# Performance work log

Hardware: AMD Instinct MI355X
Metric: run time of the kernel (lower is better)

## Reference

```python
import jax, jax.numpy as jnp
import numpy as np

NH, NKV, HD = 16, 4, 64  # num_heads, num_kv_heads, head_dim
ROPE_BASE = 10000.0


def setup_inputs() -> dict:
    key = jax.random.key(0)
    ks = jax.random.split(key, 5)
    B, S, D = 2, 2048, 1024
    x = jax.random.normal(ks[0], (B, S, D), dtype=jnp.float32)
    # torch Linear layout: [out_features, in_features], xavier-ish scale
    Wq = jax.random.normal(ks[1], (NH * HD, D), dtype=jnp.float32) * 0.02
    Wk = jax.random.normal(ks[2], (NKV * HD, D), dtype=jnp.float32) * 0.02
    Wv = jax.random.normal(ks[3], (NKV * HD, D), dtype=jnp.float32) * 0.02
    Wo = jax.random.normal(ks[4], (D, NH * HD), dtype=jnp.float32) * 0.02
    return {"x": x, "Wq": Wq, "Wk": Wk, "Wv": Wv, "Wo": Wo}


def _rotate_half(t):
    t1, t2 = jnp.split(t, 2, axis=-1)
    return jnp.concatenate([-t2, t1], axis=-1)


def _rope_cos_sin(seq_len, dtype):
    inv_freq = 1.0 / (ROPE_BASE ** (jnp.arange(0, HD, 2, dtype=jnp.float32) / HD))
    freqs = jnp.outer(jnp.arange(seq_len, dtype=jnp.float32), inv_freq)  # [S, HD/2]
    emb = jnp.concatenate([freqs, freqs], axis=-1)                       # [S, HD]
    return jnp.cos(emb).astype(dtype), jnp.sin(emb).astype(dtype)


def reference(x, Wq, Wk, Wv, Wo):
    B, S, D = x.shape
    scale = 1.0 / np.sqrt(HD)
    # projections (torch Linear: y = x @ W.T)
    q = jnp.einsum('bsd,ed->bse', x, Wq).reshape(B, S, NH, HD).transpose(0, 2, 1, 3)
    k = jnp.einsum('bsd,ed->bse', x, Wk).reshape(B, S, NKV, HD).transpose(0, 2, 1, 3)
    v = jnp.einsum('bsd,ed->bse', x, Wv).reshape(B, S, NKV, HD).transpose(0, 2, 1, 3)
    # RoPE
    cos, sin = _rope_cos_sin(S, x.dtype)
    cos = cos[None, None]  # [1,1,S,HD]
    sin = sin[None, None]
    q = q * cos + _rotate_half(q) * sin
    k = k * cos + _rotate_half(k) * sin
    # GQA: repeat kv heads (matches expand+reshape: head h = kvh*rep + r)
    rep = NH // NKV
    k = jnp.repeat(k, rep, axis=1)  # [B,NH,S,HD]
    v = jnp.repeat(v, rep, axis=1)
    # scaled dot-product attention, causal
    scores = jnp.einsum('bhqd,bhkd->bhqk', q, k) * scale
    causal = jnp.triu(jnp.ones((S, S), dtype=bool), k=1)
    scores = jnp.where(causal, jnp.float32(-jnp.inf), scores)
    attn = jax.nn.softmax(scores.astype(jnp.float32), axis=-1).astype(q.dtype)
    out = jnp.einsum('bhqk,bhkd->bhqd', attn, v)
    out = out.transpose(0, 2, 1, 3).reshape(B, S, NH * HD)
    return jnp.einsum('bse,de->bsd', out, Wo)
```

## Files before the change

### kernel.cpp

```cpp
#include <hip/hip_runtime.h>
#include <hip/hip_bf16.h>
#include <math.h>

#define B_    2
#define S_    2048
#define D_    1024
#define NH_   16
#define NKV_  4
#define HD_   64
#define NTOK  (B_ * S_)
#define QKVN  (NH_ * HD_ + 2 * NKV_ * HD_)
#define REP   (NH_ / NKV_)

typedef __attribute__((ext_vector_type(8))) short short8;
typedef __attribute__((ext_vector_type(4))) float f32x4;

__device__ short  g_xb[(size_t)NTOK * D_];
__device__ short  g_wqkv[(size_t)QKVN * D_];
__device__ short  g_wob[(size_t)D_ * NH_ * HD_];
__device__ float  g_yqkv[(size_t)NTOK * QKVN];
__device__ short  g_qb[(size_t)B_ * NH_  * S_ * HD_];
__device__ short  g_kb[(size_t)B_ * NKV_ * S_ * HD_];
__device__ short  g_vt[(size_t)B_ * NKV_ * HD_ * S_];
__device__ short  g_ao[(size_t)NTOK * NH_ * HD_];

static __device__ inline short f2bf(float f) {
  __hip_bfloat16 h = __float2bfloat16(f);
  return *reinterpret_cast<short*>(&h);
}

#define NX4   (NTOK * D_ / 4)
#define NWQ4  (NH_ * HD_ * D_ / 4)
#define NWK4  (NKV_ * HD_ * D_ / 4)
#define NWV4  NWK4
#define NWO4  (D_ * NH_ * HD_ / 4)
#define NCVT  (NX4 + NWQ4 + NWK4 + NWV4 + NWO4)

__global__ __launch_bounds__(256) void convert_all(const float* __restrict__ x,
                                                   const float* __restrict__ wq,
                                                   const float* __restrict__ wk,
                                                   const float* __restrict__ wv,
                                                   const float* __restrict__ wo) {
  int i = blockIdx.x * blockDim.x + threadIdx.x;
  if (i >= NCVT) return;
  const float* src; short* dst; int off;
  if (i < NX4)                          { src = x;  dst = g_xb;   off = i; }
  else if (i < NX4 + NWQ4)              { src = wq; dst = g_wqkv; off = i - NX4; }
  else if (i < NX4 + NWQ4 + NWK4)       { src = wk; dst = g_wqkv + (size_t)NWQ4 * 4;          off = i - NX4 - NWQ4; }
  else if (i < NX4 + NWQ4 + NWK4 + NWV4){ src = wv; dst = g_wqkv + (size_t)(NWQ4 + NWK4) * 4; off = i - NX4 - NWQ4 - NWK4; }
  else                                  { src = wo; dst = g_wob;  off = i - NX4 - NWQ4 - NWK4 - NWV4; }
  float4 v = ((const float4*)src)[off];
  short4 s;
  s.x = f2bf(v.x); s.y = f2bf(v.y); s.z = f2bf(v.z); s.w = f2bf(v.w);
  ((short4*)dst)[off] = s;
}

__global__ __launch_bounds__(256) void gemm_qkv() {
  const int w = threadIdx.x >> 6, lane = threadIdx.x & 63;
  const int m0 = blockIdx.x * 128 + w * 32;
  const int n0 = blockIdx.y * 64;
  const int lr = lane & 15, lk = (lane >> 4) * 8;

  f32x4 acc[2][4] = {};
  for (int k0 = 0; k0 < D_; k0 += 32) {
    short8 a0 = *(const short8*)(g_xb + (size_t)(m0 + lr) * D_ + k0 + lk);
    short8 a1 = *(const short8*)(g_xb + (size_t)(m0 + 16 + lr) * D_ + k0 + lk);
#pragma unroll
    for (int bj = 0; bj < 4; ++bj) {
      short8 bf = *(const short8*)(g_wqkv + (size_t)(n0 + bj * 16 + lr) * D_ + k0 + lk);
      acc[0][bj] = __builtin_amdgcn_mfma_f32_16x16x32_bf16(a0, bf, acc[0][bj], 0, 0, 0);
      acc[1][bj] = __builtin_amdgcn_mfma_f32_16x16x32_bf16(a1, bf, acc[1][bj], 0, 0, 0);
    }
  }
  const int rb = (lane >> 4) * 4;
#pragma unroll
  for (int af = 0; af < 2; ++af)
#pragma unroll
    for (int bj = 0; bj < 4; ++bj)
#pragma unroll
      for (int r = 0; r < 4; ++r)
        g_yqkv[(size_t)(m0 + af * 16 + rb + r) * QKVN + n0 + bj * 16 + lr] =
            acc[af][bj][r];
}

__global__ void rope_scatter() {
  int idx = blockIdx.x * blockDim.x + threadIdx.x;
  if (idx >= NTOK * (NH_ + NKV_) * 32) return;
  const int d    = idx & 31;
  const int head = (idx >> 5) % (NH_ + NKV_);
  const int tok  = idx / ((NH_ + NKV_) * 32);
  const int b = tok / S_, s = tok % S_;

  const float* src;
  short* dst;
  float qscale;
  if (head < NH_) {
    src = g_yqkv + (size_t)tok * QKVN + head * HD_;
    dst = g_qb + (((size_t)(b * NH_ + head)) * S_ + s) * HD_;
    qscale = 0.125f;
  } else {
    const int kvh = head - NH_;
    src = g_yqkv + (size_t)tok * QKVN + NH_ * HD_ + kvh * HD_;
    dst = g_kb + (((size_t)(b * NKV_ + kvh)) * S_ + s) * HD_;
    qscale = 1.0f;
  }
  const float x1 = src[d], x2 = src[d + 32];
  const float inv = exp2f((float)d * (-13.287712379549449f / 32.0f));
  const float ang = (float)s * inv;
  float sn, cs;
  sincosf(ang, &sn, &cs);
  dst[d]      = f2bf((x1 * cs - x2 * sn) * qscale);
  dst[d + 32] = f2bf((x2 * cs + x1 * sn) * qscale);
}

__global__ void vt_scatter() {
  int idx = blockIdx.x * blockDim.x + threadIdx.x;
  if (idx >= B_ * NKV_ * HD_ * S_) return;
  const int s   = idx & (S_ - 1);
  const int d   = (idx >> 11) & 63;
  const int kvh = (idx >> 17) & 3;
  const int b   = idx >> 19;
  const float v = g_yqkv[(size_t)(b * S_ + s) * QKVN + NH_ * HD_ + NKV_ * HD_ + kvh * HD_ + d];
  g_vt[(((size_t)(b * NKV_ + kvh)) * HD_ + d) * S_ + s] = f2bf(v);
}

__global__ __launch_bounds__(256) void attn_mfma() {
  const int bh  = blockIdx.x;
  const int b   = bh >> 4, h = bh & 15;
  const int kvh = h >> 2;
  const int qt  = (int)(gridDim.y - 1 - blockIdx.y);
  const int w   = threadIdx.x >> 6;
  const int lane = threadIdx.x & 63;
  const int g = lane >> 4, l = lane & 15;
  const int q0 = qt * 64 + w * 16;
  const int q_glob = q0 + l;

  const short* Qb = g_qb + ((size_t)bh * S_ + q0) * HD_;
  const short* Kb = g_kb + ((size_t)(b * NKV_ + kvh)) * S_ * HD_;
  const short* Vt = g_vt + ((size_t)(b * NKV_ + kvh)) * HD_ * S_;

  short8 qf[2];
  qf[0] = *(const short8*)(Qb + l * HD_ + g * 8);
  qf[1] = *(const short8*)(Qb + l * HD_ + 32 + g * 8);

  f32x4 o[4] = {};
  float m_run = -1e30f, l_run = 0.0f;

  const int nt = (q0 >> 5) + 1;
  for (int t = 0; t < nt; ++t) {
    f32x4 st[2] = {};
    const short* Kt = Kb + (size_t)(t * 32) * HD_;
#pragma unroll
    for (int ks = 0; ks < 2; ++ks) {
      short8 k0 = *(const short8*)(Kt + l * HD_ + ks * 32 + g * 8);
      short8 k1 = *(const short8*)(Kt + (16 + l) * HD_ + ks * 32 + g * 8);
      st[0] = __builtin_amdgcn_mfma_f32_16x16x32_bf16(k0, qf[ks], st[0], 0, 0, 0);
      st[1] = __builtin_amdgcn_mfma_f32_16x16x32_bf16(k1, qf[ks], st[1], 0, 0, 0);
    }
    float sv[2][4];
    float mt = -1e30f;
#pragma unroll
    for (int mf = 0; mf < 2; ++mf)
#pragma unroll
      for (int r = 0; r < 4; ++r) {
        const int kv = t * 32 + mf * 16 + g * 4 + r;
        float s = st[mf][r];
        s = (kv > q_glob) ? -1e30f : s;
        sv[mf][r] = s;
        mt = fmaxf(mt, s);
      }
    mt = fmaxf(mt, __shfl_xor(mt, 16, 64));
    mt = fmaxf(mt, __shfl_xor(mt, 32, 64));
    const float m_new = fmaxf(m_run, mt);
    const float alpha = __expf(m_run - m_new);
    float p[2][4];
    float ls = 0.0f;
#pragma unroll
    for (int mf = 0; mf < 2; ++mf)
#pragma unroll
      for (int r = 0; r < 4; ++r) {
        const float pv = __expf(sv[mf][r] - m_new);
        p[mf][r] = pv;
        ls += pv;
      }
    ls += __shfl_xor(ls, 16, 64);
    ls += __shfl_xor(ls, 32, 64);
    l_run = l_run * alpha + ls;
    m_run = m_new;
#pragma unroll
    for (int df = 0; df < 4; ++df)
#pragma unroll
      for (int r = 0; r < 4; ++r) o[df][r] *= alpha;

    short8 pt;
#pragma unroll
    for (int j = 0; j < 8; ++j) {
      const int src = l + ((lane >> 4 & 1) << 5) + ((j >> 2) << 4);
      const float v0 = __shfl(p[0][j & 3], src, 64);
      const float v1 = __shfl(p[1][j & 3], src, 64);
      pt[j] = f2bf((g & 2) ? v1 : v0);
    }
#pragma unroll
    for (int df = 0; df < 4; ++df) {
      short8 vf = *(const short8*)(Vt + (size_t)(df * 16 + l) * S_ + t * 32 + g * 8);
      o[df] = __builtin_amdgcn_mfma_f32_16x16x32_bf16(vf, pt, o[df], 0, 0, 0);
    }
  }

  const float inv_l = 1.0f / l_run;
  short* optr = g_ao + ((size_t)(b * S_ + q_glob)) * (NH_ * HD_) + h * HD_;
#pragma unroll
  for (int df = 0; df < 4; ++df) {
    short4 s4;
    s4.x = f2bf(o[df][0] * inv_l);
    s4.y = f2bf(o[df][1] * inv_l);
    s4.z = f2bf(o[df][2] * inv_l);
    s4.w = f2bf(o[df][3] * inv_l);
    *(short4*)(optr + df * 16 + g * 4) = s4;
  }
}

__global__ __launch_bounds__(256) void gemm_out(float* __restrict__ out) {
  const int w = threadIdx.x >> 6, lane = threadIdx.x & 63;
  const int m0 = blockIdx.x * 128 + w * 32;
  const int n0 = blockIdx.y * 64;
  const int lr = lane & 15, lk = (lane >> 4) * 8;
  const int K = NH_ * HD_;

  f32x4 acc[2][4] = {};
  for (int k0 = 0; k0 < K; k0 += 32) {
    short8 a0 = *(const short8*)(g_ao + (size_t)(m0 + lr) * K + k0 + lk);
    short8 a1 = *(const short8*)(g_ao + (size_t)(m0 + 16 + lr) * K + k0 + lk);
#pragma unroll
    for (int bj = 0; bj < 4; ++bj) {
      short8 bf = *(const short8*)(g_wob + (size_t)(n0 + bj * 16 + lr) * K + k0 + lk);
      acc[0][bj] = __builtin_amdgcn_mfma_f32_16x16x32_bf16(a0, bf, acc[0][bj], 0, 0, 0);
      acc[1][bj] = __builtin_amdgcn_mfma_f32_16x16x32_bf16(a1, bf, acc[1][bj], 0, 0, 0);
    }
  }
  const int rb = (lane >> 4) * 4;
#pragma unroll
  for (int af = 0; af < 2; ++af)
#pragma unroll
    for (int bj = 0; bj < 4; ++bj)
#pragma unroll
      for (int r = 0; r < 4; ++r)
        out[(size_t)(m0 + af * 16 + rb + r) * D_ + n0 + bj * 16 + lr] =
            acc[af][bj][r];
}

extern "C" void kernel_launch(void* const* d_in, const int* in_sizes, int n_in,
                              void* d_out, int out_size, void* d_ws, size_t ws_size,
                              hipStream_t stream) {
  const float* x  = (const float*)d_in[0];
  const float* Wq = (const float*)d_in[1];
  const float* Wk = (const float*)d_in[2];
  const float* Wv = (const float*)d_in[3];
  const float* Wo = (const float*)d_in[4];
  float* out = (float*)d_out;

  convert_all<<<(NCVT + 255) / 256, 256, 0, stream>>>(x, Wq, Wk, Wv, Wo);
  {
    dim3 g(NTOK / 128, QKVN / 64);
    gemm_qkv<<<g, 256, 0, stream>>>();
  }
  {
    int n = NTOK * (NH_ + NKV_) * 32;
    rope_scatter<<<(n + 255) / 256, 256, 0, stream>>>();
  }
  {
    int n = B_ * NKV_ * HD_ * S_;
    vt_scatter<<<(n + 255) / 256, 256, 0, stream>>>();
  }
  {
    dim3 g(B_ * NH_, S_ / 64);
    attn_mfma<<<g, 256, 0, stream>>>();
  }
  {
    dim3 g(NTOK / 128, D_ / 64);
    gemm_out<<<g, 256, 0, stream>>>(out);
  }
}
```

Measured before the change: 358.5 us.

## Fuse RoPE and V-transpose into QKV GEMM epilogue, restructure attention softmax

Removes the fp32 QKV intermediate buffer and the separate rope/vt scatter kernels by applying RoPE (from a precomputed cos/sin table) and writing bf16 Q, K and transposed V directly in the GEMM epilogue. The attention kernel now runs one wave per block over 16 queries. It also folds log2e into the Q scale so it can use exp2, skips the rescale when the running max has not grown by more than a threshold, defers the row-sum reduction to the end, packs P into bf16 pairs to halve the shuffles, and prefetches K/V fragments. This cuts memory traffic and launch count, at the cost of scattered epilogue stores and a slightly different numeric path from the lazy rescaling.

```diff
diff --git a/kernel.cpp b/kernel.cpp
--- a/kernel.cpp
+++ b/kernel.cpp
@@ -12,13 +12,16 @@
 #define QKVN  (NH_ * HD_ + 2 * NKV_ * HD_)
 #define REP   (NH_ / NKV_)
 
+#define LOG2E 1.4426950408889634f
+
 typedef __attribute__((ext_vector_type(8))) short short8;
 typedef __attribute__((ext_vector_type(4))) float f32x4;
 
 __device__ short  g_xb[(size_t)NTOK * D_];
 __device__ short  g_wqkv[(size_t)QKVN * D_];
 __device__ short  g_wob[(size_t)D_ * NH_ * HD_];
-__device__ float  g_yqkv[(size_t)NTOK * QKVN];
+__device__ float  g_rc[(size_t)S_ * 32];
+__device__ float  g_rs[(size_t)S_ * 32];
 __device__ short  g_qb[(size_t)B_ * NH_  * S_ * HD_];
 __device__ short  g_kb[(size_t)B_ * NKV_ * S_ * HD_];
 __device__ short  g_vt[(size_t)B_ * NKV_ * HD_ * S_];
@@ -27,6 +30,9 @@
 static __device__ inline short f2bf(float f) {
   __hip_bfloat16 h = __float2bfloat16(f);
   return *reinterpret_cast<short*>(&h);
+}
+static __device__ inline unsigned pack2(float lo, float hi) {
+  return ((unsigned)(unsigned short)f2bf(hi) << 16) | (unsigned)(unsigned short)f2bf(lo);
 }
 
 #define NX4   (NTOK * D_ / 4)
@@ -55,10 +61,22 @@
   ((short4*)dst)[off] = s;
 }
 
-__global__ __launch_bounds__(256) void gemm_qkv() {
+__global__ __launch_bounds__(256) void rope_tbl() {
+  int i = blockIdx.x * blockDim.x + threadIdx.x;
+  if (i >= S_ * 32) return;
+  const int d = i & 31, s = i >> 5;
+  const float inv = exp2f((float)d * (-13.287712379549449f / 32.0f));
+  const float ang = (float)s * inv;
+  float sn, cs;
+  sincosf(ang, &sn, &cs);
+  g_rc[i] = cs; g_rs[i] = sn;
+}
+
+__global__ __launch_bounds__(256) void gemm_qkv_rope() {
   const int w = threadIdx.x >> 6, lane = threadIdx.x & 63;
   const int m0 = blockIdx.x * 128 + w * 32;
-  const int n0 = blockIdx.y * 64;
+  const int nb = blockIdx.y;
+  const int n0 = nb * 64;
   const int lr = lane & 15, lk = (lane >> 4) * 8;
 
   f32x4 acc[2][4] = {};
@@ -73,66 +91,54 @@
     }
   }
   const int rb = (lane >> 4) * 4;
-#pragma unroll
-  for (int af = 0; af < 2; ++af)
-#pragma unroll
-    for (int bj = 0; bj < 4; ++bj)
-#pragma unroll
-      for (int r = 0; r < 4; ++r)
-        g_yqkv[(size_t)(m0 + af * 16 + rb + r) * QKVN + n0 + bj * 16 + lr] =
-            acc[af][bj][r];
-}
-
-__global__ void rope_scatter() {
-  int idx = blockIdx.x * blockDim.x + threadIdx.x;
-  if (idx >= NTOK * (NH_ + NKV_) * 32) return;
-  const int d    = idx & 31;
-  const int head = (idx >> 5) % (NH_ + NKV_);
-  const int tok  = idx / ((NH_ + NKV_) * 32);
-  const int b = tok / S_, s = tok % S_;
-
-  const float* src;
-  short* dst;
-  float qscale;
-  if (head < NH_) {
-    src = g_yqkv + (size_t)tok * QKVN + head * HD_;
-    dst = g_qb + (((size_t)(b * NH_ + head)) * S_ + s) * HD_;
-    qscale = 0.125f;
+
+  if (nb < 20) {
+    const float sc = (nb < 16) ? 0.125f * LOG2E : 1.0f;
+    short* const base = (nb < 16) ? g_qb : g_kb;
+    const int hh = (nb < 16) ? nb : (nb - 16);
+    const int nhh = (nb < 16) ? NH_ : NKV_;
+#pragma unroll
+    for (int af = 0; af < 2; ++af)
+#pragma unroll
+      for (int bj = 0; bj < 2; ++bj) {
+        const int d0 = bj * 16 + lr;
+#pragma unroll
+        for (int r = 0; r < 4; ++r) {
+          const int tok = m0 + af * 16 + rb + r;
+          const int bI = tok >> 11, s = tok & (S_ - 1);
+          const float c  = g_rc[s * 32 + d0];
+          const float sn = g_rs[s * 32 + d0];
+          const float lo = acc[af][bj][r], hi = acc[af][bj + 2][r];
+          short* dp = base + (((size_t)(bI * nhh + hh)) * S_ + s) * HD_;
+          dp[d0]      = f2bf((lo * c - hi * sn) * sc);
+          dp[d0 + 32] = f2bf((hi * c + lo * sn) * sc);
+        }
+      }
   } else {
-    const int kvh = head - NH_;
-    src = g_yqkv + (size_t)tok * QKVN + NH_ * HD_ + kvh * HD_;
-    dst = g_kb + (((size_t)(b * NKV_ + kvh)) * S_ + s) * HD_;
-    qscale = 1.0f;
-  }
-  const float x1 = src[d], x2 = src[d + 32];
-  const float inv = exp2f((float)d * (-13.287712379549449f / 32.0f));
-  const float ang = (float)s * inv;
-  float sn, cs;
-  sincosf(ang, &sn, &cs);
-  dst[d]      = f2bf((x1 * cs - x2 * sn) * qscale);
-  dst[d + 32] = f2bf((x2 * cs + x1 * sn) * qscale);
-}
-
-__global__ void vt_scatter() {
-  int idx = blockIdx.x * blockDim.x + threadIdx.x;
-  if (idx >= B_ * NKV_ * HD_ * S_) return;
-  const int s   = idx & (S_ - 1);
-  const int d   = (idx >> 11) & 63;
-  const int kvh = (idx >> 17) & 3;
-  const int b   = idx >> 19;
-  const float v = g_yqkv[(size_t)(b * S_ + s) * QKVN + NH_ * HD_ + NKV_ * HD_ + kvh * HD_ + d];
-  g_vt[(((size_t)(b * NKV_ + kvh)) * HD_ + d) * S_ + s] = f2bf(v);
-}
-
-__global__ __launch_bounds__(256) void attn_mfma() {
+    const int kvh = nb - 20;
+#pragma unroll
+    for (int af = 0; af < 2; ++af)
+#pragma unroll
+      for (int bj = 0; bj < 4; ++bj) {
+        const int d = bj * 16 + lr;
+        const int tok0 = m0 + af * 16 + rb;
+        const int bI = tok0 >> 11, s0 = tok0 & (S_ - 1);
+        short4 s4;
+        s4.x = f2bf(acc[af][bj][0]); s4.y = f2bf(acc[af][bj][1]);
+        s4.z = f2bf(acc[af][bj][2]); s4.w = f2bf(acc[af][bj][3]);
+        *(short4*)(g_vt + (((size_t)(bI * NKV_ + kvh)) * HD_ + d) * S_ + s0) = s4;
+      }
+  }
+}
+
+__global__ __launch_bounds__(64) void attn_mfma() {
   const int bh  = blockIdx.x;
   const int b   = bh >> 4, h = bh & 15;
   const int kvh = h >> 2;
-  const int qt  = (int)(gridDim.y - 1 - blockIdx.y);
-  const int w   = threadIdx.x >> 6;
-  const int lane = threadIdx.x & 63;
+  const int qw  = (int)(gridDim.y - 1 - blockIdx.y);
+  const int lane = threadIdx.x;
   const int g = lane >> 4, l = lane & 15;
-  const int q0 = qt * 64 + w * 16;
+  const int q0 = qw * 16;
   const int q_glob = q0 + l;
 
   const short* Qb = g_qb + ((size_t)bh * S_ + q0) * HD_;
@@ -144,19 +150,26 @@
   qf[1] = *(const short8*)(Qb + l * HD_ + 32 + g * 8);
 
   f32x4 o[4] = {};
-  float m_run = -1e30f, l_run = 0.0f;
+  float m_run = -1e30f, l_part = 0.0f;
 
   const int nt = (q0 >> 5) + 1;
   for (int t = 0; t < nt; ++t) {
+    const short* Kt = Kb + (size_t)(t * 32) * HD_;
+    short8 kf0 = *(const short8*)(Kt + l * HD_ + g * 8);
+    short8 kf1 = *(const short8*)(Kt + (16 + l) * HD_ + g * 8);
+    short8 kf2 = *(const short8*)(Kt + l * HD_ + 32 + g * 8);
+    short8 kf3 = *(const short8*)(Kt + (16 + l) * HD_ + 32 + g * 8);
+    short8 vf[4];
+#pragma unroll
+    for (int df = 0; df < 4; ++df)
+      vf[df] = *(const short8*)(Vt + (size_t)(df * 16 + l) * S_ + t * 32 + g * 8);
+
     f32x4 st[2] = {};
-    const short* Kt = Kb + (size_t)(t * 32) * HD_;
-#pragma unroll
-    for (int ks = 0; ks < 2; ++ks) {
-      short8 k0 = *(const short8*)(Kt + l * HD_ + ks * 32 + g * 8);
-      short8 k1 = *(const short8*)(Kt + (16 + l) * HD_ + ks * 32 + g * 8);
-      st[0] = __builtin_amdgcn_mfma_f32_16x16x32_bf16(k0, qf[ks], st[0], 0, 0, 0);
-      st[1] = __builtin_amdgcn_mfma_f32_16x16x32_bf16(k1, qf[ks], st[1], 0, 0, 0);
-    }
+    st[0] = __builtin_amdgcn_mfma_f32_16x16x32_bf16(kf0, qf[0], st[0], 0, 0, 0);
+    st[1] = __builtin_amdgcn_mfma_f32_16x16x32_bf16(kf1, qf[0], st[1], 0, 0, 0);
+    st[0] = __builtin_amdgcn_mfma_f32_16x16x32_bf16(kf2, qf[1], st[0], 0, 0, 0);
+    st[1] = __builtin_amdgcn_mfma_f32_16x16x32_bf16(kf3, qf[1], st[1], 0, 0, 0);
+
     float sv[2][4];
     float mt = -1e30f;
 #pragma unroll
@@ -169,45 +182,53 @@
         sv[mf][r] = s;
         mt = fmaxf(mt, s);
       }
-    mt = fmaxf(mt, __shfl_xor(mt, 16, 64));
-    mt = fmaxf(mt, __shfl_xor(mt, 32, 64));
-    const float m_new = fmaxf(m_run, mt);
-    const float alpha = __expf(m_run - m_new);
+    if (__any(mt > m_run + 8.0f)) {
+      float mr = mt;
+      mr = fmaxf(mr, __shfl_xor(mr, 16, 64));
+      mr = fmaxf(mr, __shfl_xor(mr, 32, 64));
+      const float m_new = fmaxf(m_run, mr);
+      const float alpha = exp2f(m_run - m_new);
+      l_part *= alpha;
+#pragma unroll
+      for (int df = 0; df < 4; ++df)
+#pragma unroll
+        for (int r = 0; r < 4; ++r) o[df][r] *= alpha;
+      m_run = m_new;
+    }
     float p[2][4];
-    float ls = 0.0f;
 #pragma unroll
     for (int mf = 0; mf < 2; ++mf)
 #pragma unroll
       for (int r = 0; r < 4; ++r) {
-        const float pv = __expf(sv[mf][r] - m_new);
+        const float pv = exp2f(sv[mf][r] - m_run);
         p[mf][r] = pv;
-        ls += pv;
-      }
-    ls += __shfl_xor(ls, 16, 64);
-    ls += __shfl_xor(ls, 32, 64);
-    l_run = l_run * alpha + ls;
-    m_run = m_new;
+        l_part += pv;
+      }
+    unsigned u0 = pack2(p[0][0], p[0][1]);
+    unsigned u1 = pack2(p[0][2], p[0][3]);
+    unsigned u2 = pack2(p[1][0], p[1][1]);
+    unsigned u3 = pack2(p[1][2], p[1][3]);
+    const int srcA = ((g & 1) << 5) + l;
+    const int srcB = srcA + 16;
+    const unsigned a0 = __shfl(u0, srcA, 64), a2 = __shfl(u2, srcA, 64);
+    const unsigned b1 = __shfl(u1, srcA, 64), b3 = __shfl(u3, srcA, 64);
+    const unsigned c0 = __shfl(u0, srcB, 64), c2 = __shfl(u2, srcB, 64);
+    const unsigned d1 = __shfl(u1, srcB, 64), d3 = __shfl(u3, srcB, 64);
+    const bool hi = (g & 2);
+    unsigned W[4];
+    W[0] = hi ? a2 : a0;  W[1] = hi ? b3 : b1;
+    W[2] = hi ? c2 : c0;  W[3] = hi ? d3 : d1;
+    short8 pt = *reinterpret_cast<short8*>(W);
+
 #pragma unroll
     for (int df = 0; df < 4; ++df)
-#pragma unroll
-      for (int r = 0; r < 4; ++r) o[df][r] *= alpha;
-
-    short8 pt;
-#pragma unroll
-    for (int j = 0; j < 8; ++j) {
-      const int src = l + ((lane >> 4 & 1) << 5) + ((j >> 2) << 4);
-      const float v0 = __shfl(p[0][j & 3], src, 64);
-      const float v1 = __shfl(p[1][j & 3], src, 64);
-      pt[j] = f2bf((g & 2) ? v1 : v0);
-    }
-#pragma unroll
-    for (int df = 0; df < 4; ++df) {
-      short8 vf = *(const short8*)(Vt + (size_t)(df * 16 + l) * S_ + t * 32 + g * 8);
-      o[df] = __builtin_amdgcn_mfma_f32_16x16x32_bf16(vf, pt, o[df], 0, 0, 0);
-    }
-  }
-
-  const float inv_l = 1.0f / l_run;
+      o[df] = __builtin_amdgcn_mfma_f32_16x16x32_bf16(vf[df], pt, o[df], 0, 0, 0);
+  }
+
+  float l1 = l_part + __shfl_xor(l_part, 16, 64);
+  const float l_tot = l1 + __shfl_xor(l1, 32, 64);
+  const float inv_l = 1.0f / l_tot;
+
   short* optr = g_ao + ((size_t)(b * S_ + q_glob)) * (NH_ * HD_) + h * HD_;
 #pragma unroll
   for (int df = 0; df < 4; ++df) {
@@ -260,21 +281,14 @@
   float* out = (float*)d_out;
 
   convert_all<<<(NCVT + 255) / 256, 256, 0, stream>>>(x, Wq, Wk, Wv, Wo);
+  rope_tbl<<<(S_ * 32 + 255) / 256, 256, 0, stream>>>();
   {
     dim3 g(NTOK / 128, QKVN / 64);
-    gemm_qkv<<<g, 256, 0, stream>>>();
+    gemm_qkv_rope<<<g, 256, 0, stream>>>();
   }
   {
-    int n = NTOK * (NH_ + NKV_) * 32;
-    rope_scatter<<<(n + 255) / 256, 256, 0, stream>>>();
-  }
-  {
-    int n = B_ * NKV_ * HD_ * S_;
-    vt_scatter<<<(n + 255) / 256, 256, 0, stream>>>();
-  }
-  {
-    dim3 g(B_ * NH_, S_ / 64);
-    attn_mfma<<<g, 256, 0, stream>>>();
+    dim3 g(B_ * NH_, S_ / 16);
+    attn_mfma<<<g, 64, 0, stream>>>();
   }
   {
     dim3 g(NTOK / 128, D_ / 64);
```

Measured after the change: 327.1 us. -8.8%, faster.
